# Performance work log

Measured on AMD Instinct MI355X. Metric: run time of the kernel, lower is better.

The kernel has to match this reference:

```python
import jax, jax.numpy as jnp
import numpy as np

NUM_HEADS = 16
SIZE_PER_HEAD = 64
NEG_INF = -10000.0

def setup_inputs() -> dict:
    key = jax.random.key(0)
    ks = jax.random.split(key, 4)
    B, S, D = 4, 2048, 1024
    x = jax.random.normal(ks[0], (B, S, D), dtype=jnp.float32)
    mask = jnp.ones((B, S), dtype=jnp.int32)
    std = 0.02
    Wq = jax.random.normal(ks[1], (D, NUM_HEADS * SIZE_PER_HEAD), dtype=jnp.float32) * std
    Wk = jax.random.normal(ks[2], (D, NUM_HEADS * SIZE_PER_HEAD), dtype=jnp.float32) * std
    Wv = jax.random.normal(ks[3], (D, NUM_HEADS * SIZE_PER_HEAD), dtype=jnp.float32) * std
    bq = jnp.zeros((NUM_HEADS * SIZE_PER_HEAD,), dtype=jnp.float32)
    bk = jnp.zeros((NUM_HEADS * SIZE_PER_HEAD,), dtype=jnp.float32)
    bv = jnp.zeros((NUM_HEADS * SIZE_PER_HEAD,), dtype=jnp.float32)
    return {"x": x, "mask": mask, "Wq": Wq, "bq": bq, "Wk": Wk, "bk": bk, "Wv": Wv, "bv": bv}

def reference(x, mask, Wq, bq, Wk, bk, Wv, bv):
    B, S, D = x.shape
    H, Dh = NUM_HEADS, SIZE_PER_HEAD
    # QKV projections (no activations: query/key/value_activation default None)
    q = (x @ Wq + bq).reshape(B, S, H, Dh).transpose(0, 2, 1, 3)  # [B,H,S,Dh]
    k = (x @ Wk + bk).reshape(B, S, H, Dh).transpose(0, 2, 1, 3)
    v = (x @ Wv + bv).reshape(B, S, H, Dh).transpose(0, 2, 1, 3)
    scores = jnp.einsum('bhqd,bhkd->bhqk', q, k) / jnp.sqrt(jnp.float32(Dh))  # [B,H,S,S]
    # additive mask: (1 - mask) * neg_inf, broadcast over heads and query dim
    adder = (1.0 - mask.astype(jnp.float32))[:, None, None, :] * NEG_INF
    probs = jax.nn.softmax(scores + adder, axis=-1)
    # dropout is identity at inference (training=None)
    ctx = jnp.einsum('bhqk,bhkd->bhqd', probs, v)  # [B,H,S,Dh]
    return ctx.transpose(0, 2, 1, 3).reshape(B, S, H * Dh)
```

## Files before the change

kernel.cpp:

```cpp
#include <hip/hip_runtime.h>


typedef __attribute__((ext_vector_type(8))) short bf16x8;
typedef __attribute__((ext_vector_type(4))) float f32x4;
typedef __attribute__((ext_vector_type(16))) float f32x16;

#define LOG2E 1.4426950408889634f

__device__ __forceinline__ ushort f2bf(float f) {
  union { float f; unsigned int u; } x; x.f = f;
  unsigned int r = x.u + 0x7fffu + ((x.u >> 16) & 1u);
  return (ushort)(r >> 16);
}

__device__ __forceinline__ void gload16(const ushort* g, ushort* l) {
  __builtin_amdgcn_global_load_lds(
      (__attribute__((address_space(1))) unsigned int*)(g),
      (__attribute__((address_space(3))) unsigned int*)(l), 16, 0, 0);
}

__global__ __launch_bounds__(256) void prep(
    const float* __restrict__ x, ushort* __restrict__ xb,
    const float* __restrict__ Wq, const float* __restrict__ Wk,
    const float* __restrict__ Wv, ushort* __restrict__ WT,
    const int* __restrict__ mask, int* __restrict__ flagw) {
  __shared__ float tile[32][33];
  __shared__ int accum[64];
  const int blk = blockIdx.x, t = threadIdx.x;
  if (blk < 8192) {
    int i = blk * 256 + t;
    float4 v = ((const float4*)x)[i];
    ushort4 o;
    o.x = f2bf(v.x); o.y = f2bf(v.y); o.z = f2bf(v.z); o.w = f2bf(v.w);
    ((ushort4*)xb)[i] = o;
  } else if (blk < 11264) {
    int bb = blk - 8192;
    int z = bb >> 10, rem = bb & 1023, db = rem >> 5, nb = rem & 31;
    const float* W = (z == 0) ? Wq : ((z == 1) ? Wk : Wv);
    int tx = t & 31, ty = t >> 5;
#pragma unroll
    for (int i = 0; i < 4; i++) {
      int dl = ty + i * 8;
      tile[dl][tx] = W[(size_t)(db * 32 + dl) * 1024 + nb * 32 + tx];
    }
    __syncthreads();
#pragma unroll
    for (int i = 0; i < 4; i++) {
      int nl = ty + i * 8;
      WT[(size_t)(z * 1024 + nb * 32 + nl) * 1024 + db * 32 + tx] = f2bf(tile[tx][nl]);
    }
  } else {
    if (t < 64) accum[t] = 0;
    __syncthreads();
    int p = t >> 2, j = t & 3;
    int base = p * 128 + j * 32;
    int s = 0;
#pragma unroll
    for (int i = 0; i < 8; i++) {
      int4 v = *(const int4*)(mask + base + i * 4);
      s += v.x + v.y + v.z + v.w;
    }
    atomicAdd(&accum[p], s);
    __syncthreads();
    if (t < 4) {
      int w = 0;
#pragma unroll
      for (int kt = 0; kt < 16; kt++)
        if (accum[t * 16 + kt] != 128) w |= (1 << kt);
      flagw[t] = w;
    }
  }
}

__global__ __launch_bounds__(256, 2) void gemm_qkv(
    const ushort* __restrict__ xb, const ushort* __restrict__ WT,
    const float* __restrict__ bq, const float* __restrict__ bk,
    const float* __restrict__ bv, ushort* __restrict__ Qg,
    ushort* __restrict__ Kg, ushort* __restrict__ VTg) {
  __shared__ __align__(16) ushort As[128 * 64];
  __shared__ __align__(16) ushort Bs[128 * 64];
  const int t = threadIdx.x, wid = t >> 6, lane = t & 63;
  const int blk = blockIdx.x;
  int mode, mb, nb;
  const ushort *A, *B;
  if (blk < 1024) {
    mode = 0;
    int lin2 = (blk & 7) * 128 + (blk >> 3);
    nb = lin2 & 15; mb = lin2 >> 4;
    A = xb; B = WT;
  } else {
    mode = 1;
    int l = blk - 1024;
    int lin2 = (l & 7) * 64 + (l >> 3);
    mb = lin2 & 7; nb = lin2 >> 3;
    A = WT + (size_t)2048 * 1024; B = xb;
  }
  const ushort* Ab = A + (size_t)mb * 128 * 1024;
  const ushort* Bb = B + (size_t)nb * 128 * 1024;
  const int wr = wid >> 1, wc = wid & 1;

  f32x4 acc[4][4] = {};

  const int srow = lane >> 3;
  const int schunk = (lane & 7) ^ srow;

#pragma unroll
  for (int i = 0; i < 4; i++) {
    int blki = i * 4 + wid;
    int row = blki * 8 + srow;
    int ldso = __builtin_amdgcn_readfirstlane(blki * 512);
    gload16(Ab + (size_t)row * 1024 + schunk * 8, As + ldso);
    gload16(Bb + (size_t)row * 1024 + schunk * 8, Bs + ldso);
  }

  for (int kt = 0; kt < 16; ++kt) {
    __syncthreads();

    bf16x8 af[2][4], bf[2][4];
#pragma unroll
    for (int ks = 0; ks < 2; ks++) {
#pragma unroll
      for (int m = 0; m < 4; m++) {
        int row = wr * 64 + m * 16 + (lane & 15);
        int slot = (ks * 4 + (lane >> 4)) ^ (row & 7);
        af[ks][m] = *(const bf16x8*)(As + row * 64 + slot * 8);
      }
#pragma unroll
      for (int n = 0; n < 4; n++) {
        int row = wc * 64 + n * 16 + (lane & 15);
        int slot = (ks * 4 + (lane >> 4)) ^ (row & 7);
        bf[ks][n] = *(const bf16x8*)(Bs + row * 64 + slot * 8);
      }
    }
    __syncthreads();

    if (kt < 15) {
      const int kof = (kt + 1) * 64 + schunk * 8;
#pragma unroll
      for (int i = 0; i < 4; i++) {
        int blki = i * 4 + wid;
        int row = blki * 8 + srow;
        int ldso = __builtin_amdgcn_readfirstlane(blki * 512);
        gload16(Ab + (size_t)row * 1024 + kof, As + ldso);
        gload16(Bb + (size_t)row * 1024 + kof, Bs + ldso);
      }
    }

#pragma unroll
    for (int ks = 0; ks < 2; ks++)
#pragma unroll
      for (int m = 0; m < 4; m++)
#pragma unroll
        for (int n = 0; n < 4; n++)
          acc[m][n] = __builtin_amdgcn_mfma_f32_16x16x32_bf16(
              af[ks][m], bf[ks][n], acc[m][n], 0, 0, 0);
  }

#pragma unroll
  for (int m = 0; m < 4; m++) {
#pragma unroll
    for (int n = 0; n < 4; n++) {
      if (mode == 0) {
        int col = nb * 128 + wc * 64 + n * 16 + (lane & 15);
        int wq = col >> 10;
        float bs = wq ? bk[col & 1023] : bq[col & 1023];
        float scale = wq ? 1.0f : (0.125f * LOG2E);
        ushort* dst = wq ? Kg : Qg;
        int h = (col >> 6) & 15, d = col & 63;
#pragma unroll
        for (int r = 0; r < 4; r++) {
          int row = mb * 128 + wr * 64 + m * 16 + (lane >> 4) * 4 + r;
          int b = row >> 11, s = row & 2047;
          float v = (acc[m][n][r] + bs) * scale;
          dst[((size_t)((b << 4) + h) * 2048 + s) * 64 + d] = f2bf(v);
        }
      } else {
        int col = nb * 128 + wc * 64 + n * 16 + (lane & 15);
        int b = col >> 11, s = col & 2047;
#pragma unroll
        for (int r = 0; r < 4; r++) {
          int p = mb * 128 + wr * 64 + m * 16 + (lane >> 4) * 4 + r;
          float v = acc[m][n][r] + bv[p];
          int h = p >> 6, d = p & 63;
          VTg[((size_t)((b << 4) + h) * 64 + d) * 2048 + s] = f2bf(v);
        }
      }
    }
  }
}

__global__ __launch_bounds__(256, 3) void attn_kernel(
    const ushort* __restrict__ Qg, const ushort* __restrict__ Kg,
    const ushort* __restrict__ VTg, const int* __restrict__ mask,
    const int* __restrict__ flagw, float* __restrict__ out) {
  __shared__ __align__(16) ushort Ks[128 * 64];
  __shared__ __align__(16) ushort Vs[64 * 128];
  __shared__ float maddv[128];

  const int t = threadIdx.x, wid = t >> 6, lane = t & 63;
  const int l31 = lane & 31, hi = lane >> 5;
  const int lin = blockIdx.x;
  const int lin2 = (lin & 7) * 128 + (lin >> 3);
  const int qb = lin2 & 15, bh = lin2 >> 4;
  const int b = bh >> 4, h = bh & 15;
  const ushort* Qbh = Qg + ((size_t)bh * 2048 + qb * 128) * 64;
  const ushort* Kbh = Kg + (size_t)bh * 2048 * 64;
  const ushort* Vbh = VTg + (size_t)bh * 64 * 2048;

  const int pr_l = lane >> 4;
  const int s_l = lane & 15;

  const int prq = l31 >> 1;
  const int halfq = l31 & 1;
  const int pr14 = prq & 15;

#pragma unroll
  for (int i = 0; i < 4; i++) {
    int blki = i * 4 + wid;
    int ldso = __builtin_amdgcn_readfirstlane(blki * 512);
    int pr = blki * 4 + pr_l;
    int sp = s_l ^ (pr & 15);
    gload16(Qbh + (size_t)(2 * pr + (sp >> 3)) * 64 + (sp & 7) * 8, Ks + ldso);
  }
  const int fb = flagw[b];
  __syncthreads();
  bf16x8 qf[4];
  {
    const ushort* qbase = Ks + (wid * 16 + prq) * 128;
#pragma unroll
    for (int ds = 0; ds < 4; ds++) {
      int slot = ((ds * 2 + hi) | (halfq << 3)) ^ pr14;
      qf[ds] = *(const bf16x8*)(qbase + slot * 8);
    }
  }
  __syncthreads();

  const f32x16 fzero = {};
  f32x16 cacc[2] = {};
  float l0 = 0.f, l1 = 0.f, l2 = 0.f, l3 = 0.f;

  for (int kt = 0; kt < 16; ++kt) {
    {
#pragma unroll
      for (int i = 0; i < 4; i++) {
        int blki = i * 4 + wid;
        int ldso = __builtin_amdgcn_readfirstlane(blki * 512);
        int pr = blki * 4 + pr_l;
        int sp = s_l ^ (pr & 15);
        gload16(Kbh + (size_t)(kt * 128 + 2 * pr + (sp >> 3)) * 64 + (sp & 7) * 8,
                Ks + ldso);
      }
      int d_l = lane >> 4, c_s = lane & 15;
#pragma unroll
      for (int i = 0; i < 4; i++) {
        int blki = i * 4 + wid;
        int ldso = __builtin_amdgcn_readfirstlane(blki * 512);
        int d = blki * 4 + d_l;
        int cvg = c_s ^ (d & 15);
        gload16(Vbh + (size_t)d * 2048 + kt * 128 + cvg * 8, Vs + ldso);
      }
    }
    const bool msk = ((fb >> kt) & 1) != 0;
    if (msk && t < 128)
      maddv[t] = (1.0f - (float)mask[b * 2048 + kt * 128 + t]) * (-10000.0f * LOG2E);
    __syncthreads();

#pragma unroll
    for (int kb = 0; kb < 4; kb++) {
      const ushort* krow = Ks + (kb * 16 + prq) * 128;
      __builtin_amdgcn_s_setprio(1);
      bf16x8 kf0 = *(const bf16x8*)(krow + (((0 + hi) | (halfq << 3)) ^ pr14) * 8);
      f32x16 a = __builtin_amdgcn_mfma_f32_32x32x16_bf16(kf0, qf[0], fzero, 0, 0, 0);
      bf16x8 kf1 = *(const bf16x8*)(krow + (((2 + hi) | (halfq << 3)) ^ pr14) * 8);
      a = __builtin_amdgcn_mfma_f32_32x32x16_bf16(kf1, qf[1], a, 0, 0, 0);
      bf16x8 kf2 = *(const bf16x8*)(krow + (((4 + hi) | (halfq << 3)) ^ pr14) * 8);
      a = __builtin_amdgcn_mfma_f32_32x32x16_bf16(kf2, qf[2], a, 0, 0, 0);
      bf16x8 kf3 = *(const bf16x8*)(krow + (((6 + hi) | (halfq << 3)) ^ pr14) * 8);
      a = __builtin_amdgcn_mfma_f32_32x32x16_bf16(kf3, qf[3], a, 0, 0, 0);
      __builtin_amdgcn_s_setprio(0);

      if (msk) {
#pragma unroll
        for (int qd = 0; qd < 4; qd++) {
          f32x4 ma = *(const f32x4*)(maddv + kb * 32 + qd * 8 + hi * 4);
#pragma unroll
          for (int rr = 0; rr < 4; rr++) a[qd * 4 + rr] += ma[rr];
        }
      }

#pragma unroll
      for (int w2 = 0; w2 < 2; w2++) {
        const int o = w2 * 8;
        float e0 = __builtin_amdgcn_exp2f(a[o + 0]);
        float e1 = __builtin_amdgcn_exp2f(a[o + 1]);
        float e2 = __builtin_amdgcn_exp2f(a[o + 2]);
        float e3 = __builtin_amdgcn_exp2f(a[o + 3]);
        float e4 = __builtin_amdgcn_exp2f(a[o + 4]);
        float e5 = __builtin_amdgcn_exp2f(a[o + 5]);
        float e6 = __builtin_amdgcn_exp2f(a[o + 6]);
        float e7 = __builtin_amdgcn_exp2f(a[o + 7]);
        l0 += e0; l1 += e1; l2 += e2; l3 += e3;
        l0 += e4; l1 += e5; l2 += e6; l3 += e7;
        unsigned a0, a1, b0, b1;
        asm("v_cvt_pk_bf16_f32 %0, %1, %2" : "=v"(a0) : "v"(e0), "v"(e1));
        asm("v_cvt_pk_bf16_f32 %0, %1, %2" : "=v"(a1) : "v"(e2), "v"(e3));
        asm("v_cvt_pk_bf16_f32 %0, %1, %2" : "=v"(b0) : "v"(e4), "v"(e5));
        asm("v_cvt_pk_bf16_f32 %0, %1, %2" : "=v"(b1) : "v"(e6), "v"(e7));
        asm("v_permlane32_swap_b32 %0, %1" : "+v"(a0), "+v"(b0));
        asm("v_permlane32_swap_b32 %0, %1" : "+v"(a1), "+v"(b1));
        union { unsigned u[4]; bf16x8 v8; } pu;
        pu.u[0] = a0; pu.u[1] = a1; pu.u[2] = b0; pu.u[3] = b1;
        bf16x8 pf = pu.v8;
        int w = kb * 2 + w2;
        __builtin_amdgcn_s_setprio(1);
#pragma unroll
        for (int df = 0; df < 2; df++) {
          int d = df * 32 + l31;
          int c = (w * 2 + hi) ^ (d & 15);
          bf16x8 vf = *(const bf16x8*)(Vs + d * 128 + c * 8);
          cacc[df] = __builtin_amdgcn_mfma_f32_32x32x16_bf16(vf, pf, cacc[df], 0, 0, 0);
        }
        __builtin_amdgcn_s_setprio(0);
      }
    }
    __syncthreads();
  }

  float lrun = (l0 + l1) + (l2 + l3);
  lrun += __shfl_xor(lrun, 32);
  float linv = 1.0f / lrun;
  int qg = qb * 128 + wid * 32 + l31;
  float* op = out + ((size_t)(b * 2048 + qg)) * 1024 + h * 64;
#pragma unroll
  for (int df = 0; df < 2; df++)
#pragma unroll
    for (int qd = 0; qd < 4; qd++) {
      f32x4 v;
      v[0] = cacc[df][qd * 4 + 0] * linv;
      v[1] = cacc[df][qd * 4 + 1] * linv;
      v[2] = cacc[df][qd * 4 + 2] * linv;
      v[3] = cacc[df][qd * 4 + 3] * linv;
      *(f32x4*)(op + df * 32 + qd * 8 + hi * 4) = v;
    }
}

extern "C" void kernel_launch(void* const* d_in, const int* in_sizes, int n_in,
                              void* d_out, int out_size, void* d_ws, size_t ws_size,
                              hipStream_t stream) {
  const float* x  = (const float*)d_in[0];
  const int* mask = (const int*)d_in[1];
  const float* Wq = (const float*)d_in[2];
  const float* bq = (const float*)d_in[3];
  const float* Wk = (const float*)d_in[4];
  const float* bk = (const float*)d_in[5];
  const float* Wv = (const float*)d_in[6];
  const float* bv = (const float*)d_in[7];
  float* out = (float*)d_out;

  char* ws = (char*)d_ws;
  ushort* xb  = (ushort*)(ws);
  ushort* WT  = (ushort*)(ws + (size_t)16777216);
  ushort* Qg  = (ushort*)(ws + (size_t)23068672);
  ushort* Kg  = (ushort*)(ws + (size_t)39845888);
  ushort* VTg = (ushort*)(ws + (size_t)56623104);
  int*    flg = (int*)(ws + (size_t)73400320);

  prep<<<dim3(11265), dim3(256), 0, stream>>>(x, xb, Wq, Wk, Wv, WT, mask, flg);
  gemm_qkv<<<dim3(1536), dim3(256), 0, stream>>>(xb, WT, bq, bk, bv, Qg, Kg, VTg);
  attn_kernel<<<dim3(1024), dim3(256), 0, stream>>>(Qg, Kg, VTg, mask, flg, out);
}
```

Baseline: 155.9 us.

## Double query tile per block to reuse K/V tiles across 256 queries

Each attention block now handles 256 query rows instead of 128, with each wave owning two 32-row query sub-tiles that share every K and V fragment read from LDS. This halves the grid and halves the global and LDS traffic for K/V per query. Q fragments are loaded straight from global into registers instead of staging through LDS, and the final-iteration barrier is skipped. The cost is higher register use (occupancy hint lowered to 2) and fewer blocks for the 256 CUs.

```diff
diff --git a/kernel.cpp b/kernel.cpp
--- a/kernel.cpp
+++ b/kernel.cpp
@@ -189,7 +189,7 @@
   }
 }
 
-__global__ __launch_bounds__(256, 3) void attn_kernel(
+__global__ __launch_bounds__(256, 2) void attn_kernel(
     const ushort* __restrict__ Qg, const ushort* __restrict__ Kg,
     const ushort* __restrict__ VTg, const int* __restrict__ mask,
     const int* __restrict__ flagw, float* __restrict__ out) {
@@ -200,10 +200,10 @@
   const int t = threadIdx.x, wid = t >> 6, lane = t & 63;
   const int l31 = lane & 31, hi = lane >> 5;
   const int lin = blockIdx.x;
-  const int lin2 = (lin & 7) * 128 + (lin >> 3);
-  const int qb = lin2 & 15, bh = lin2 >> 4;
+  const int lin2 = (lin & 7) * 64 + (lin >> 3);
+  const int qb = lin2 & 7, bh = lin2 >> 3;
   const int b = bh >> 4, h = bh & 15;
-  const ushort* Qbh = Qg + ((size_t)bh * 2048 + qb * 128) * 64;
+  const ushort* Qbh = Qg + ((size_t)bh * 2048 + qb * 256) * 64;
   const ushort* Kbh = Kg + (size_t)bh * 2048 * 64;
   const ushort* Vbh = VTg + (size_t)bh * 64 * 2048;
 
@@ -214,51 +214,33 @@
   const int halfq = l31 & 1;
   const int pr14 = prq & 15;
 
-#pragma unroll
-  for (int i = 0; i < 4; i++) {
-    int blki = i * 4 + wid;
-    int ldso = __builtin_amdgcn_readfirstlane(blki * 512);
-    int pr = blki * 4 + pr_l;
-    int sp = s_l ^ (pr & 15);
-    gload16(Qbh + (size_t)(2 * pr + (sp >> 3)) * 64 + (sp & 7) * 8, Ks + ldso);
+  bf16x8 qf[2][4];
+#pragma unroll
+  for (int qh = 0; qh < 2; qh++) {
+    const ushort* qrow = Qbh + (size_t)(wid * 64 + qh * 32 + l31) * 64 + hi * 8;
+#pragma unroll
+    for (int ds = 0; ds < 4; ds++)
+      qf[qh][ds] = *(const bf16x8*)(qrow + ds * 16);
   }
   const int fb = flagw[b];
-  __syncthreads();
-  bf16x8 qf[4];
-  {
-    const ushort* qbase = Ks + (wid * 16 + prq) * 128;
-#pragma unroll
-    for (int ds = 0; ds < 4; ds++) {
-      int slot = ((ds * 2 + hi) | (halfq << 3)) ^ pr14;
-      qf[ds] = *(const bf16x8*)(qbase + slot * 8);
-    }
-  }
-  __syncthreads();
 
   const f32x16 fzero = {};
-  f32x16 cacc[2] = {};
-  float l0 = 0.f, l1 = 0.f, l2 = 0.f, l3 = 0.f;
+  f32x16 cacc[2][2] = {};
+  float lsA0 = 0.f, lsA1 = 0.f, lsA2 = 0.f, lsA3 = 0.f;
+  float lsB0 = 0.f, lsB1 = 0.f, lsB2 = 0.f, lsB3 = 0.f;
 
   for (int kt = 0; kt < 16; ++kt) {
-    {
-#pragma unroll
-      for (int i = 0; i < 4; i++) {
-        int blki = i * 4 + wid;
-        int ldso = __builtin_amdgcn_readfirstlane(blki * 512);
-        int pr = blki * 4 + pr_l;
-        int sp = s_l ^ (pr & 15);
-        gload16(Kbh + (size_t)(kt * 128 + 2 * pr + (sp >> 3)) * 64 + (sp & 7) * 8,
-                Ks + ldso);
-      }
-      int d_l = lane >> 4, c_s = lane & 15;
-#pragma unroll
-      for (int i = 0; i < 4; i++) {
-        int blki = i * 4 + wid;
-        int ldso = __builtin_amdgcn_readfirstlane(blki * 512);
-        int d = blki * 4 + d_l;
-        int cvg = c_s ^ (d & 15);
-        gload16(Vbh + (size_t)d * 2048 + kt * 128 + cvg * 8, Vs + ldso);
-      }
+#pragma unroll
+    for (int i = 0; i < 4; i++) {
+      int blki = i * 4 + wid;
+      int ldso = __builtin_amdgcn_readfirstlane(blki * 512);
+      int pr = blki * 4 + pr_l;
+      int sp = s_l ^ (pr & 15);
+      gload16(Kbh + (size_t)(kt * 128 + 2 * pr + (sp >> 3)) * 64 + (sp & 7) * 8,
+              Ks + ldso);
+      int d = blki * 4 + pr_l;
+      int cvg = s_l ^ (d & 15);
+      gload16(Vbh + (size_t)d * 2048 + kt * 128 + cvg * 8, Vs + ldso);
     }
     const bool msk = ((fb >> kt) & 1) != 0;
     if (msk && t < 128)
@@ -270,13 +252,17 @@
       const ushort* krow = Ks + (kb * 16 + prq) * 128;
       __builtin_amdgcn_s_setprio(1);
       bf16x8 kf0 = *(const bf16x8*)(krow + (((0 + hi) | (halfq << 3)) ^ pr14) * 8);
-      f32x16 a = __builtin_amdgcn_mfma_f32_32x32x16_bf16(kf0, qf[0], fzero, 0, 0, 0);
+      f32x16 aA = __builtin_amdgcn_mfma_f32_32x32x16_bf16(kf0, qf[0][0], fzero, 0, 0, 0);
+      f32x16 aB = __builtin_amdgcn_mfma_f32_32x32x16_bf16(kf0, qf[1][0], fzero, 0, 0, 0);
       bf16x8 kf1 = *(const bf16x8*)(krow + (((2 + hi) | (halfq << 3)) ^ pr14) * 8);
-      a = __builtin_amdgcn_mfma_f32_32x32x16_bf16(kf1, qf[1], a, 0, 0, 0);
+      aA = __builtin_amdgcn_mfma_f32_32x32x16_bf16(kf1, qf[0][1], aA, 0, 0, 0);
+      aB = __builtin_amdgcn_mfma_f32_32x32x16_bf16(kf1, qf[1][1], aB, 0, 0, 0);
       bf16x8 kf2 = *(const bf16x8*)(krow + (((4 + hi) | (halfq << 3)) ^ pr14) * 8);
-      a = __builtin_amdgcn_mfma_f32_32x32x16_bf16(kf2, qf[2], a, 0, 0, 0);
+      aA = __builtin_amdgcn_mfma_f32_32x32x16_bf16(kf2, qf[0][2], aA, 0, 0, 0);
+      aB = __builtin_amdgcn_mfma_f32_32x32x16_bf16(kf2, qf[1][2], aB, 0, 0, 0);
       bf16x8 kf3 = *(const bf16x8*)(krow + (((6 + hi) | (halfq << 3)) ^ pr14) * 8);
-      a = __builtin_amdgcn_mfma_f32_32x32x16_bf16(kf3, qf[3], a, 0, 0, 0);
+      aA = __builtin_amdgcn_mfma_f32_32x32x16_bf16(kf3, qf[0][3], aA, 0, 0, 0);
+      aB = __builtin_amdgcn_mfma_f32_32x32x16_bf16(kf3, qf[1][3], aB, 0, 0, 0);
       __builtin_amdgcn_s_setprio(0);
 
       if (msk) {
@@ -284,64 +270,94 @@
         for (int qd = 0; qd < 4; qd++) {
           f32x4 ma = *(const f32x4*)(maddv + kb * 32 + qd * 8 + hi * 4);
 #pragma unroll
-          for (int rr = 0; rr < 4; rr++) a[qd * 4 + rr] += ma[rr];
+          for (int rr = 0; rr < 4; rr++) {
+            aA[qd * 4 + rr] += ma[rr];
+            aB[qd * 4 + rr] += ma[rr];
+          }
         }
       }
 
 #pragma unroll
       for (int w2 = 0; w2 < 2; w2++) {
         const int o = w2 * 8;
-        float e0 = __builtin_amdgcn_exp2f(a[o + 0]);
-        float e1 = __builtin_amdgcn_exp2f(a[o + 1]);
-        float e2 = __builtin_amdgcn_exp2f(a[o + 2]);
-        float e3 = __builtin_amdgcn_exp2f(a[o + 3]);
-        float e4 = __builtin_amdgcn_exp2f(a[o + 4]);
-        float e5 = __builtin_amdgcn_exp2f(a[o + 5]);
-        float e6 = __builtin_amdgcn_exp2f(a[o + 6]);
-        float e7 = __builtin_amdgcn_exp2f(a[o + 7]);
-        l0 += e0; l1 += e1; l2 += e2; l3 += e3;
-        l0 += e4; l1 += e5; l2 += e6; l3 += e7;
-        unsigned a0, a1, b0, b1;
-        asm("v_cvt_pk_bf16_f32 %0, %1, %2" : "=v"(a0) : "v"(e0), "v"(e1));
-        asm("v_cvt_pk_bf16_f32 %0, %1, %2" : "=v"(a1) : "v"(e2), "v"(e3));
-        asm("v_cvt_pk_bf16_f32 %0, %1, %2" : "=v"(b0) : "v"(e4), "v"(e5));
-        asm("v_cvt_pk_bf16_f32 %0, %1, %2" : "=v"(b1) : "v"(e6), "v"(e7));
-        asm("v_permlane32_swap_b32 %0, %1" : "+v"(a0), "+v"(b0));
-        asm("v_permlane32_swap_b32 %0, %1" : "+v"(a1), "+v"(b1));
-        union { unsigned u[4]; bf16x8 v8; } pu;
-        pu.u[0] = a0; pu.u[1] = a1; pu.u[2] = b0; pu.u[3] = b1;
-        bf16x8 pf = pu.v8;
-        int w = kb * 2 + w2;
+        float eA0 = __builtin_amdgcn_exp2f(aA[o + 0]);
+        float eA1 = __builtin_amdgcn_exp2f(aA[o + 1]);
+        float eA2 = __builtin_amdgcn_exp2f(aA[o + 2]);
+        float eA3 = __builtin_amdgcn_exp2f(aA[o + 3]);
+        float eA4 = __builtin_amdgcn_exp2f(aA[o + 4]);
+        float eA5 = __builtin_amdgcn_exp2f(aA[o + 5]);
+        float eA6 = __builtin_amdgcn_exp2f(aA[o + 6]);
+        float eA7 = __builtin_amdgcn_exp2f(aA[o + 7]);
+        lsA0 += eA0; lsA1 += eA1; lsA2 += eA2; lsA3 += eA3;
+        lsA0 += eA4; lsA1 += eA5; lsA2 += eA6; lsA3 += eA7;
+        unsigned pA0, pA1, pA2, pA3;
+        asm("v_cvt_pk_bf16_f32 %0, %1, %2" : "=v"(pA0) : "v"(eA0), "v"(eA1));
+        asm("v_cvt_pk_bf16_f32 %0, %1, %2" : "=v"(pA1) : "v"(eA2), "v"(eA3));
+        asm("v_cvt_pk_bf16_f32 %0, %1, %2" : "=v"(pA2) : "v"(eA4), "v"(eA5));
+        asm("v_cvt_pk_bf16_f32 %0, %1, %2" : "=v"(pA3) : "v"(eA6), "v"(eA7));
+        asm("v_permlane32_swap_b32 %0, %1" : "+v"(pA0), "+v"(pA2));
+        asm("v_permlane32_swap_b32 %0, %1" : "+v"(pA1), "+v"(pA3));
+        union { unsigned u[4]; bf16x8 v8; } puA;
+        puA.u[0] = pA0; puA.u[1] = pA1; puA.u[2] = pA2; puA.u[3] = pA3;
+        bf16x8 pfA = puA.v8;
+        float eB0 = __builtin_amdgcn_exp2f(aB[o + 0]);
+        float eB1 = __builtin_amdgcn_exp2f(aB[o + 1]);
+        float eB2 = __builtin_amdgcn_exp2f(aB[o + 2]);
+        float eB3 = __builtin_amdgcn_exp2f(aB[o + 3]);
+        float eB4 = __builtin_amdgcn_exp2f(aB[o + 4]);
+        float eB5 = __builtin_amdgcn_exp2f(aB[o + 5]);
+        float eB6 = __builtin_amdgcn_exp2f(aB[o + 6]);
+        float eB7 = __builtin_amdgcn_exp2f(aB[o + 7]);
+        lsB0 += eB0; lsB1 += eB1; lsB2 += eB2; lsB3 += eB3;
+        lsB0 += eB4; lsB1 += eB5; lsB2 += eB6; lsB3 += eB7;
+        unsigned pB0, pB1, pB2, pB3;
+        asm("v_cvt_pk_bf16_f32 %0, %1, %2" : "=v"(pB0) : "v"(eB0), "v"(eB1));
+        asm("v_cvt_pk_bf16_f32 %0, %1, %2" : "=v"(pB1) : "v"(eB2), "v"(eB3));
+        asm("v_cvt_pk_bf16_f32 %0, %1, %2" : "=v"(pB2) : "v"(eB4), "v"(eB5));
+        asm("v_cvt_pk_bf16_f32 %0, %1, %2" : "=v"(pB3) : "v"(eB6), "v"(eB7));
+        asm("v_permlane32_swap_b32 %0, %1" : "+v"(pB0), "+v"(pB2));
+        asm("v_permlane32_swap_b32 %0, %1" : "+v"(pB1), "+v"(pB3));
+        union { unsigned u[4]; bf16x8 v8; } puB;
+        puB.u[0] = pB0; puB.u[1] = pB1; puB.u[2] = pB2; puB.u[3] = pB3;
+        bf16x8 pfB = puB.v8;
+
+        const int w = kb * 2 + w2;
         __builtin_amdgcn_s_setprio(1);
 #pragma unroll
         for (int df = 0; df < 2; df++) {
           int d = df * 32 + l31;
           int c = (w * 2 + hi) ^ (d & 15);
           bf16x8 vf = *(const bf16x8*)(Vs + d * 128 + c * 8);
-          cacc[df] = __builtin_amdgcn_mfma_f32_32x32x16_bf16(vf, pf, cacc[df], 0, 0, 0);
+          cacc[df][0] = __builtin_amdgcn_mfma_f32_32x32x16_bf16(vf, pfA, cacc[df][0], 0, 0, 0);
+          cacc[df][1] = __builtin_amdgcn_mfma_f32_32x32x16_bf16(vf, pfB, cacc[df][1], 0, 0, 0);
         }
         __builtin_amdgcn_s_setprio(0);
       }
     }
-    __syncthreads();
-  }
-
-  float lrun = (l0 + l1) + (l2 + l3);
-  lrun += __shfl_xor(lrun, 32);
-  float linv = 1.0f / lrun;
-  int qg = qb * 128 + wid * 32 + l31;
-  float* op = out + ((size_t)(b * 2048 + qg)) * 1024 + h * 64;
-#pragma unroll
-  for (int df = 0; df < 2; df++)
-#pragma unroll
-    for (int qd = 0; qd < 4; qd++) {
-      f32x4 v;
-      v[0] = cacc[df][qd * 4 + 0] * linv;
-      v[1] = cacc[df][qd * 4 + 1] * linv;
-      v[2] = cacc[df][qd * 4 + 2] * linv;
-      v[3] = cacc[df][qd * 4 + 3] * linv;
-      *(f32x4*)(op + df * 32 + qd * 8 + hi * 4) = v;
-    }
+
+    if (kt < 15) __syncthreads();
+  }
+
+#pragma unroll
+  for (int qh = 0; qh < 2; qh++) {
+    float lrun = qh ? ((lsB0 + lsB1) + (lsB2 + lsB3))
+                    : ((lsA0 + lsA1) + (lsA2 + lsA3));
+    lrun += __shfl_xor(lrun, 32);
+    float linv = 1.0f / lrun;
+    int qg = qb * 256 + wid * 64 + qh * 32 + l31;
+    float* op = out + ((size_t)(b * 2048 + qg)) * 1024 + h * 64;
+#pragma unroll
+    for (int df = 0; df < 2; df++)
+#pragma unroll
+      for (int qd = 0; qd < 4; qd++) {
+        f32x4 v;
+        v[0] = cacc[df][qh][qd * 4 + 0] * linv;
+        v[1] = cacc[df][qh][qd * 4 + 1] * linv;
+        v[2] = cacc[df][qh][qd * 4 + 2] * linv;
+        v[3] = cacc[df][qh][qd * 4 + 3] * linv;
+        *(f32x4*)(op + df * 32 + qd * 8 + hi * 4) = v;
+      }
+  }
 }
 
 extern "C" void kernel_launch(void* const* d_in, const int* in_sizes, int n_in,
@@ -367,5 +383,5 @@
 
   prep<<<dim3(11265), dim3(256), 0, stream>>>(x, xb, Wq, Wk, Wv, WT, mask, flg);
   gemm_qkv<<<dim3(1536), dim3(256), 0, stream>>>(xb, WT, bq, bk, bv, Qg, Kg, VTg);
-  attn_kernel<<<dim3(1024), dim3(256), 0, stream>>>(Qg, Kg, VTg, mask, flg, out);
-}
+  attn_kernel<<<dim3(512), dim3(256), 0, stream>>>(Qg, Kg, VTg, mask, flg, out);
+}
```

Measured after the change: 180.7 us. +15.9%, slower.
